# Performance work log

Hardware: AMD Instinct MI355X
Metric: run time of the kernel (lower is better)

The kernel has to match this reference:

```python
import jax, jax.numpy as jnp
import numpy as np

QMAX = 127.0          # int8 clip bound (symmetric, preserve-zero)
QDIV = 127.5          # AQT int8 scale divisor: 2**(bits-1) - 0.5


def _safe(s):
    # avoid div-by-zero for all-zero rows/cols
    return jnp.where(s == 0.0, 1.0, s)


def setup_inputs() -> dict:
    key = jax.random.key(0)
    k1, k2 = jax.random.split(key)
    lhs = jax.random.normal(k1, (8192, 4096), dtype=jnp.float32)
    rhs = jax.random.normal(k2, (4096, 4096), dtype=jnp.float32)
    return {"lhs": lhs, "rhs": rhs}


def reference(lhs, rhs):
    # --- dynamic symmetric int8 quantization (AQT abs-max calibration) ---
    # lhs: contract over axis 1 -> per-row scale [M, 1]
    s_l = _safe(jnp.max(jnp.abs(lhs), axis=1, keepdims=True) / QDIV)
    # rhs: contract over axis 0 -> per-column scale [1, N]
    s_r = _safe(jnp.max(jnp.abs(rhs), axis=0, keepdims=True) / QDIV)

    q_l = jnp.clip(jnp.round(lhs / s_l), -QMAX, QMAX).astype(jnp.int8)
    q_r = jnp.clip(jnp.round(rhs / s_r), -QMAX, QMAX).astype(jnp.int8)

    # --- integer matmul with int32 accumulation ---
    acc = jax.lax.dot_general(
        q_l, q_r,
        dimension_numbers=(((1,), (0,)), ((), ())),
        preferred_element_type=jnp.int32,
    )

    # --- dequantize: outer product of per-row / per-column scales ---
    return acc.astype(jnp.float32) * s_l * s_r
```

## Files before the change

kernel.cpp:

```cpp
#include <hip/hip_runtime.h>
#include <stdint.h>

#define M_DIM 8192
#define N_DIM 4096
#define K_DIM 4096
#define QMAXF 127.0f
#define QDIVF 127.5f

typedef int v4i  __attribute__((ext_vector_type(4)));
typedef int v16i __attribute__((ext_vector_type(16)));

typedef __attribute__((address_space(3))) void lds_void_t;
typedef __attribute__((address_space(1))) const void glb_void_t;

static __device__ __forceinline__ void load_lds16(const void* g, void* l) {
    __builtin_amdgcn_global_load_lds((glb_void_t*)g, (lds_void_t*)l, 16, 0, 0);
}

__global__ __launch_bounds__(256) void prep1_kernel(
        const float* __restrict__ lhs, const float* __restrict__ rhs,
        float* __restrict__ sL, unsigned* __restrict__ bits,
        int8_t* __restrict__ ql) {
    const int t = threadIdx.x;
    if (blockIdx.x < M_DIM) {
        const int row = blockIdx.x;
        const float4* rp = (const float4*)(lhs + (size_t)row * K_DIM);
        float4 v[4];
        float m = 0.0f;
#pragma unroll
        for (int i = 0; i < 4; ++i) {
            v[i] = rp[t + i * 256];
            m = fmaxf(m, fmaxf(fmaxf(fabsf(v[i].x), fabsf(v[i].y)),
                               fmaxf(fabsf(v[i].z), fabsf(v[i].w))));
        }
#pragma unroll
        for (int off = 32; off; off >>= 1) m = fmaxf(m, __shfl_down(m, off, 64));
        __shared__ float wmax[4];
        if ((t & 63) == 0) wmax[t >> 6] = m;
        __syncthreads();
        const float mm = fmaxf(fmaxf(wmax[0], wmax[1]), fmaxf(wmax[2], wmax[3]));
        float s = mm / QDIVF;
        s = (s == 0.0f) ? 1.0f : s;
        if (t == 0) sL[row] = s;
        unsigned* qo = (unsigned*)ql + (size_t)row * 1024;
#pragma unroll
        for (int i = 0; i < 4; ++i) {
            int q0 = (int)fminf(fmaxf(rintf(v[i].x / s), -QMAXF), QMAXF);
            int q1 = (int)fminf(fmaxf(rintf(v[i].y / s), -QMAXF), QMAXF);
            int q2 = (int)fminf(fmaxf(rintf(v[i].z / s), -QMAXF), QMAXF);
            int q3 = (int)fminf(fmaxf(rintf(v[i].w / s), -QMAXF), QMAXF);
            qo[t + i * 256] = (q0 & 255) | ((q1 & 255) << 8) | ((q2 & 255) << 16)
                            | ((unsigned)(q3 & 255) << 24);
        }
    } else {
        const int cb = blockIdx.x - M_DIM;
        const int col = (cb & 15) * 256 + t;
        const int r0 = (cb >> 4) * 64;
        float m = 0.0f;
#pragma unroll 4
        for (int r = 0; r < 64; ++r)
            m = fmaxf(m, fabsf(rhs[(size_t)(r0 + r) * N_DIM + col]));
        atomicMax(&bits[col], __float_as_uint(m));
    }
}

__global__ __launch_bounds__(256) void quant_rhs_t_kernel(
        const float* __restrict__ rhs, const unsigned* __restrict__ bits,
        float* __restrict__ sR, int8_t* __restrict__ qbT) {
    __shared__ __align__(16) int8_t lt[64][80];
    const int n0 = blockIdx.x * 64;
    const int k0 = blockIdx.y * 64;
    const int t = threadIdx.x;
    const int nloc = t & 63;
    const int kq = (t >> 6) * 16;
    float s = __uint_as_float(bits[n0 + nloc]) / QDIVF;
    s = (s == 0.0f) ? 1.0f : s;
    if (blockIdx.y == 0 && t < 64) sR[n0 + t] = (__uint_as_float(bits[n0 + t]) / QDIVF == 0.0f)
                                               ? 1.0f : __uint_as_float(bits[n0 + t]) / QDIVF;
#pragma unroll
    for (int i = 0; i < 4; ++i) {
        unsigned pack = 0;
#pragma unroll
        for (int j = 0; j < 4; ++j) {
            int kk = kq + i * 4 + j;
            float x = rhs[(size_t)(k0 + kk) * N_DIM + n0 + nloc];
            int q = (int)fminf(fmaxf(rintf(x / s), -QMAXF), QMAXF);
            pack |= (unsigned)(q & 255) << (8 * j);
        }
        *(unsigned*)&lt[nloc][kq + i * 4] = pack;
    }
    __syncthreads();
    const int nn = t >> 2, ch = t & 3;
    v4i val = *(const v4i*)&lt[nn][ch * 16];
    *(v4i*)&qbT[(size_t)(n0 + nn) * K_DIM + k0 + ch * 16] = val;
}


#define BAR() do { asm volatile("" ::: "memory");          \
                   __builtin_amdgcn_s_barrier();           \
                   asm volatile("" ::: "memory"); } while (0)

#define VMCNT(N) asm volatile("s_waitcnt vmcnt(%0)" :: "n"(N) : "memory")

#define STAGE_A(h, kt, bq) \
    load_lds16(gA0 + (size_t)((h) * 128) * K_DIM + (size_t)(kt) * 64, \
               lds + (bq) * 16384 + (h) * 8192 + sdst)
#define STAGE_B(h, kt, bq) \
    load_lds16(gB0 + (size_t)((h) * 128) * K_DIM + (size_t)(kt) * 64, \
               lds + 65536 + (bq) * 16384 + (h) * 8192 + sdst)

#define RD_A(BUF, MF, KS) (*(const v4i*)(lds + (BUF) * 16384 + aoff[MF][KS]))
#define RD_B(BUF, NF, KS) (*(const v4i*)(lds + (BUF) * 16384 + boff[NF][KS]))

#define TILE(KT, BUF, P, S, VM, RDN) do {                                       \
    _Pragma("unroll") for (int mf = 0; mf < 2; ++mf) a1[mf] = RD_A(BUF, mf, 1); \
    _Pragma("unroll") for (int nf = 0; nf < 4; ++nf) b1[nf] = RD_B(BUF, nf, 1); \
    if (S) { STAGE_A(0, (KT) + 3, ((BUF) + 3) & 3);                             \
             STAGE_A(1, (KT) + 3, ((BUF) + 3) & 3);                             \
             STAGE_B(0, (KT) + 3, ((BUF) + 3) & 3);                             \
             STAGE_B(1, (KT) + 3, ((BUF) + 3) & 3); }                           \
    __builtin_amdgcn_s_setprio(1);                                              \
    _Pragma("unroll") for (int mf = 0; mf < 2; ++mf)                            \
    _Pragma("unroll") for (int nf = 0; nf < 4; ++nf)                            \
        acc[mf][nf] = __builtin_amdgcn_mfma_i32_32x32x32_i8(                    \
            a0[P][mf], b0[P][nf], acc[mf][nf], 0, 0, 0);                        \
    __builtin_amdgcn_s_setprio(0);                                              \
    if (RDN) {                                                                  \
        _Pragma("unroll") for (int mf = 0; mf < 2; ++mf)                        \
            a0[(P) ^ 1][mf] = RD_A(((BUF) + 1) & 3, mf, 0);                     \
        _Pragma("unroll") for (int nf = 0; nf < 4; ++nf)                        \
            b0[(P) ^ 1][nf] = RD_B(((BUF) + 1) & 3, nf, 0);                     \
    }                                                                           \
    __builtin_amdgcn_s_setprio(1);                                              \
    _Pragma("unroll") for (int mf = 0; mf < 2; ++mf)                            \
    _Pragma("unroll") for (int nf = 0; nf < 4; ++nf)                            \
        acc[mf][nf] = __builtin_amdgcn_mfma_i32_32x32x32_i8(                    \
            a1[mf], b1[nf], acc[mf][nf], 0, 0, 0);                              \
    __builtin_amdgcn_s_setprio(0);                                              \
    VMCNT(VM);                                                                  \
    BAR();                                                                      \
} while (0)

__global__ __launch_bounds__(512, 2) void gemm_i8_kernel(
        const int8_t* __restrict__ qa, const int8_t* __restrict__ qbT,
        const float* __restrict__ sL, const float* __restrict__ sR,
        float* __restrict__ out) {
    __shared__ __align__(16) int8_t lds[131072];

    const int t = threadIdx.x;
    const int wave = t >> 6;
    const int lane = t & 63;

    const int bid = blockIdx.x;
    const int xcd = bid & 7;
    const int idx = bid >> 3;
    const int mt = (xcd >> 1) * 8 + (idx & 7);
    const int nt = (xcd & 1) * 8 + (idx >> 3);
    const int brow = mt * 256;
    const int bcol = nt * 256;

    const int wm = (wave >> 1) * 64;
    const int wn = (wave & 1) * 128;

    int aoff[2][2], boff[4][2];
#pragma unroll
    for (int mf = 0; mf < 2; ++mf) {
        int row = wm + mf * 32 + (lane & 31);
#pragma unroll
        for (int ks = 0; ks < 2; ++ks)
            aoff[mf][ks] = row * 64 + (((ks * 2 + (lane >> 5)) ^ ((row >> 1) & 3)) * 16);
    }
#pragma unroll
    for (int nf = 0; nf < 4; ++nf) {
        int row = wn + nf * 32 + (lane & 31);
#pragma unroll
        for (int ks = 0; ks < 2; ++ks)
            boff[nf][ks] = 65536 + row * 64 + (((ks * 2 + (lane >> 5)) ^ ((row >> 1) & 3)) * 16);
    }

    v16i acc[2][4];
#pragma unroll
    for (int mf = 0; mf < 2; ++mf)
#pragma unroll
        for (int nf = 0; nf < 4; ++nf) acc[mf][nf] = (v16i)(0);

    const int srow = t >> 2;
    const int lcA = (t & 3) ^ ((srow >> 1) & 3);
    const int8_t* gA0 = qa  + (size_t)(brow + srow) * K_DIM + lcA * 16;
    const int8_t* gB0 = qbT + (size_t)(bcol + srow) * K_DIM + lcA * 16;
    const int sdst = t * 16;

    v4i a0[2][2], b0[2][4], a1[2], b1[4];

    STAGE_A(0, 0, 0); STAGE_A(1, 0, 0); STAGE_B(0, 0, 0); STAGE_B(1, 0, 0);
    STAGE_A(0, 1, 1); STAGE_A(1, 1, 1); STAGE_B(0, 1, 1); STAGE_B(1, 1, 1);
    STAGE_A(0, 2, 2); STAGE_A(1, 2, 2); STAGE_B(0, 2, 2); STAGE_B(1, 2, 2);
    VMCNT(4);
    BAR();
#pragma unroll
    for (int mf = 0; mf < 2; ++mf) a0[0][mf] = RD_A(0, mf, 0);
#pragma unroll
    for (int nf = 0; nf < 4; ++nf) b0[0][nf] = RD_B(0, nf, 0);

    for (int kt = 0; kt < 60; kt += 4) {
        TILE(kt + 0, 0, 0, 1, 4, 1);
        TILE(kt + 1, 1, 1, 1, 4, 1);
        TILE(kt + 2, 2, 0, 1, 4, 1);
        TILE(kt + 3, 3, 1, 1, 4, 1);
    }
    TILE(60, 0, 0, 1, 4, 1);
    TILE(61, 1, 1, 0, 0, 1);
    TILE(62, 2, 0, 0, 0, 1);
    TILE(63, 3, 1, 0, 0, 0);

    const int cc = lane & 31;
    const int lh = (lane >> 5) * 4;
#pragma unroll
    for (int mf = 0; mf < 2; ++mf) {
        const int rbase = brow + wm + mf * 32 + lh;
        float slv[16];
#pragma unroll
        for (int q = 0; q < 4; ++q)
#pragma unroll
            for (int j = 0; j < 4; ++j)
                slv[q * 4 + j] = sL[rbase + q * 8 + j];
#pragma unroll
        for (int nf = 0; nf < 4; ++nf) {
            const int gcol = bcol + wn + nf * 32 + cc;
            const float sc = sR[gcol];
#pragma unroll
            for (int q = 0; q < 4; ++q)
#pragma unroll
                for (int j = 0; j < 4; ++j) {
                    const int grow = rbase + q * 8 + j;
                    out[(size_t)grow * N_DIM + gcol] =
                        (float)acc[mf][nf][q * 4 + j] * slv[q * 4 + j] * sc;
                }
        }
    }
}

extern "C" void kernel_launch(void* const* d_in, const int* in_sizes, int n_in,
                              void* d_out, int out_size, void* d_ws, size_t ws_size,
                              hipStream_t stream) {
    const float* lhs = (const float*)d_in[0];
    const float* rhs = (const float*)d_in[1];
    float* out = (float*)d_out;

    uint8_t* ws = (uint8_t*)d_ws;
    int8_t* ql    = (int8_t*)ws;
    int8_t* qbT   = (int8_t*)(ws + 33554432);
    float* sL     = (float*)(ws + 50331648);
    float* sR     = (float*)(ws + 50331648 + 32768);
    unsigned* bits = (unsigned*)(ws + 50331648 + 32768 + 16384);

    hipMemsetAsync(bits, 0, N_DIM * sizeof(unsigned), stream);

    prep1_kernel<<<M_DIM + 1024, 256, 0, stream>>>(lhs, rhs, sL, bits, ql);
    quant_rhs_t_kernel<<<dim3(N_DIM / 64, K_DIM / 64), 256, 0, stream>>>(
        rhs, bits, sR, qbT);
    gemm_i8_kernel<<<dim3((M_DIM / 256) * (N_DIM / 256)), 512, 0, stream>>>(
        ql, qbT, sL, sR, out);
}
```

Baseline: 219.2 us.

## Restructure int8 GEMM to K=128 tiles with double-buffered LDS pipeline

Replaces the four-stage K=64 LDS ring with a two-buffer scheme that uses K=128 tiles (64 KB per stage). Each tile now gets one wait and barrier instead of one per K=64 step, and the next tile's global-to-LDS loads are spread between the four MFMA groups. The LDS swizzle is widened to an 8-chunk XOR for 128-byte rows. The trade-off is a shallower prefetch (one tile ahead, with a full vmcnt(0) wait) in exchange for half as many barriers. A small sR computation cleanup is included.

```diff
diff --git a/kernel.cpp b/kernel.cpp
--- a/kernel.cpp
+++ b/kernel.cpp
@@ -75,8 +75,10 @@
     const int kq = (t >> 6) * 16;
     float s = __uint_as_float(bits[n0 + nloc]) / QDIVF;
     s = (s == 0.0f) ? 1.0f : s;
-    if (blockIdx.y == 0 && t < 64) sR[n0 + t] = (__uint_as_float(bits[n0 + t]) / QDIVF == 0.0f)
-                                               ? 1.0f : __uint_as_float(bits[n0 + t]) / QDIVF;
+    if (blockIdx.y == 0 && t < 64) {
+        float ss = __uint_as_float(bits[n0 + t]) / QDIVF;
+        sR[n0 + t] = (ss == 0.0f) ? 1.0f : ss;
+    }
 #pragma unroll
     for (int i = 0; i < 4; ++i) {
         unsigned pack = 0;
@@ -102,43 +104,43 @@
 
 #define VMCNT(N) asm volatile("s_waitcnt vmcnt(%0)" :: "n"(N) : "memory")
 
-#define STAGE_A(h, kt, bq) \
-    load_lds16(gA0 + (size_t)((h) * 128) * K_DIM + (size_t)(kt) * 64, \
-               lds + (bq) * 16384 + (h) * 8192 + sdst)
-#define STAGE_B(h, kt, bq) \
-    load_lds16(gB0 + (size_t)((h) * 128) * K_DIM + (size_t)(kt) * 64, \
-               lds + 65536 + (bq) * 16384 + (h) * 8192 + sdst)
-
-#define RD_A(BUF, MF, KS) (*(const v4i*)(lds + (BUF) * 16384 + aoff[MF][KS]))
-#define RD_B(BUF, NF, KS) (*(const v4i*)(lds + (BUF) * 16384 + boff[NF][KS]))
-
-#define TILE(KT, BUF, P, S, VM, RDN) do {                                       \
-    _Pragma("unroll") for (int mf = 0; mf < 2; ++mf) a1[mf] = RD_A(BUF, mf, 1); \
-    _Pragma("unroll") for (int nf = 0; nf < 4; ++nf) b1[nf] = RD_B(BUF, nf, 1); \
-    if (S) { STAGE_A(0, (KT) + 3, ((BUF) + 3) & 3);                             \
-             STAGE_A(1, (KT) + 3, ((BUF) + 3) & 3);                             \
-             STAGE_B(0, (KT) + 3, ((BUF) + 3) & 3);                             \
-             STAGE_B(1, (KT) + 3, ((BUF) + 3) & 3); }                           \
+#define STG_A(KT, BQ, H) \
+    load_lds16(gA0 + (size_t)((H) * 64) * K_DIM + (size_t)(KT) * 128, \
+               lds + (BQ) * 65536 + (H) * 8192 + sdst)
+#define STG_B(KT, BQ, H) \
+    load_lds16(gB0 + (size_t)((H) * 64) * K_DIM + (size_t)(KT) * 128, \
+               lds + (BQ) * 65536 + 32768 + (H) * 8192 + sdst)
+
+#define RD_KS(AF, BF, BUF, KS) do {                                             \
+    _Pragma("unroll") for (int mf = 0; mf < 2; ++mf)                            \
+        AF[mf] = *(const v4i*)(lds + (BUF) * 65536 + aoff[mf][KS]);             \
+    _Pragma("unroll") for (int nf = 0; nf < 4; ++nf)                            \
+        BF[nf] = *(const v4i*)(lds + (BUF) * 65536 + boff[nf][KS]);             \
+} while (0)
+
+#define MFMAC(AF, BF)                                                           \
     __builtin_amdgcn_s_setprio(1);                                              \
     _Pragma("unroll") for (int mf = 0; mf < 2; ++mf)                            \
     _Pragma("unroll") for (int nf = 0; nf < 4; ++nf)                            \
         acc[mf][nf] = __builtin_amdgcn_mfma_i32_32x32x32_i8(                    \
-            a0[P][mf], b0[P][nf], acc[mf][nf], 0, 0, 0);                        \
-    __builtin_amdgcn_s_setprio(0);                                              \
-    if (RDN) {                                                                  \
-        _Pragma("unroll") for (int mf = 0; mf < 2; ++mf)                        \
-            a0[(P) ^ 1][mf] = RD_A(((BUF) + 1) & 3, mf, 0);                     \
-        _Pragma("unroll") for (int nf = 0; nf < 4; ++nf)                        \
-            b0[(P) ^ 1][nf] = RD_B(((BUF) + 1) & 3, nf, 0);                     \
-    }                                                                           \
-    __builtin_amdgcn_s_setprio(1);                                              \
-    _Pragma("unroll") for (int mf = 0; mf < 2; ++mf)                            \
-    _Pragma("unroll") for (int nf = 0; nf < 4; ++nf)                            \
-        acc[mf][nf] = __builtin_amdgcn_mfma_i32_32x32x32_i8(                    \
-            a1[mf], b1[nf], acc[mf][nf], 0, 0, 0);                              \
-    __builtin_amdgcn_s_setprio(0);                                              \
-    VMCNT(VM);                                                                  \
+            AF[mf], BF[nf], acc[mf][nf], 0, 0, 0);                              \
+    __builtin_amdgcn_s_setprio(0);
+
+#define TILE32(KT, BUF, S) do {                                                 \
+    VMCNT(0);                                                                   \
     BAR();                                                                      \
+    RD_KS(a0, b0, BUF, 0);                                                      \
+    if (S) { STG_A((KT) + 1, (BUF) ^ 1, 0); STG_A((KT) + 1, (BUF) ^ 1, 1); }    \
+    RD_KS(a1, b1, BUF, 1);                                                      \
+    MFMAC(a0, b0);                                                              \
+    if (S) { STG_A((KT) + 1, (BUF) ^ 1, 2); STG_A((KT) + 1, (BUF) ^ 1, 3); }    \
+    RD_KS(a0, b0, BUF, 2);                                                      \
+    MFMAC(a1, b1);                                                              \
+    if (S) { STG_B((KT) + 1, (BUF) ^ 1, 0); STG_B((KT) + 1, (BUF) ^ 1, 1); }    \
+    RD_KS(a1, b1, BUF, 3);                                                      \
+    MFMAC(a0, b0);                                                              \
+    if (S) { STG_B((KT) + 1, (BUF) ^ 1, 2); STG_B((KT) + 1, (BUF) ^ 1, 3); }    \
+    MFMAC(a1, b1);                                                              \
 } while (0)
 
 __global__ __launch_bounds__(512, 2) void gemm_i8_kernel(
@@ -162,20 +164,20 @@
     const int wm = (wave >> 1) * 64;
     const int wn = (wave & 1) * 128;
 
-    int aoff[2][2], boff[4][2];
+    int aoff[2][4], boff[4][4];
 #pragma unroll
     for (int mf = 0; mf < 2; ++mf) {
         int row = wm + mf * 32 + (lane & 31);
 #pragma unroll
-        for (int ks = 0; ks < 2; ++ks)
-            aoff[mf][ks] = row * 64 + (((ks * 2 + (lane >> 5)) ^ ((row >> 1) & 3)) * 16);
+        for (int ks = 0; ks < 4; ++ks)
+            aoff[mf][ks] = row * 128 + (((ks * 2 + (lane >> 5)) ^ (row & 7)) * 16);
     }
 #pragma unroll
     for (int nf = 0; nf < 4; ++nf) {
         int row = wn + nf * 32 + (lane & 31);
 #pragma unroll
-        for (int ks = 0; ks < 2; ++ks)
-            boff[nf][ks] = 65536 + row * 64 + (((ks * 2 + (lane >> 5)) ^ ((row >> 1) & 3)) * 16);
+        for (int ks = 0; ks < 4; ++ks)
+            boff[nf][ks] = 32768 + row * 128 + (((ks * 2 + (lane >> 5)) ^ (row & 7)) * 16);
     }
 
     v16i acc[2][4];
@@ -184,34 +186,23 @@
 #pragma unroll
         for (int nf = 0; nf < 4; ++nf) acc[mf][nf] = (v16i)(0);
 
-    const int srow = t >> 2;
-    const int lcA = (t & 3) ^ ((srow >> 1) & 3);
+    const int srow = t >> 3;
+    const int lcA = (t & 7) ^ (srow & 7);
     const int8_t* gA0 = qa  + (size_t)(brow + srow) * K_DIM + lcA * 16;
     const int8_t* gB0 = qbT + (size_t)(bcol + srow) * K_DIM + lcA * 16;
     const int sdst = t * 16;
 
-    v4i a0[2][2], b0[2][4], a1[2], b1[4];
-
-    STAGE_A(0, 0, 0); STAGE_A(1, 0, 0); STAGE_B(0, 0, 0); STAGE_B(1, 0, 0);
-    STAGE_A(0, 1, 1); STAGE_A(1, 1, 1); STAGE_B(0, 1, 1); STAGE_B(1, 1, 1);
-    STAGE_A(0, 2, 2); STAGE_A(1, 2, 2); STAGE_B(0, 2, 2); STAGE_B(1, 2, 2);
-    VMCNT(4);
-    BAR();
-#pragma unroll
-    for (int mf = 0; mf < 2; ++mf) a0[0][mf] = RD_A(0, mf, 0);
-#pragma unroll
-    for (int nf = 0; nf < 4; ++nf) b0[0][nf] = RD_B(0, nf, 0);
-
-    for (int kt = 0; kt < 60; kt += 4) {
-        TILE(kt + 0, 0, 0, 1, 4, 1);
-        TILE(kt + 1, 1, 1, 1, 4, 1);
-        TILE(kt + 2, 2, 0, 1, 4, 1);
-        TILE(kt + 3, 3, 1, 1, 4, 1);
-    }
-    TILE(60, 0, 0, 1, 4, 1);
-    TILE(61, 1, 1, 0, 0, 1);
-    TILE(62, 2, 0, 0, 0, 1);
-    TILE(63, 3, 1, 0, 0, 0);
+    v4i a0[2], b0[4], a1[2], b1[4];
+
+    STG_A(0, 0, 0); STG_A(0, 0, 1); STG_A(0, 0, 2); STG_A(0, 0, 3);
+    STG_B(0, 0, 0); STG_B(0, 0, 1); STG_B(0, 0, 2); STG_B(0, 0, 3);
+
+    for (int kt = 0; kt < 30; kt += 2) {
+        TILE32(kt + 0, 0, 1);
+        TILE32(kt + 1, 1, 1);
+    }
+    TILE32(30, 0, 1);
+    TILE32(31, 1, 0);
 
     const int cc = lane & 31;
     const int lh = (lane >> 5) * 4;
```

After: 222.0 us. No clear change (+1.3%).
